# Performance work log

Measured on AMD Instinct MI355X. Metric: run time of the kernel, lower is better.

Reference implementation:

```python
import jax, jax.numpy as jnp
import numpy as np

D_MODEL, N_HEADS, D_FF, CTX_DIM = 512, 8, 2048, 20
D_K = D_MODEL // N_HEADS
SCALE = float(np.sqrt(D_K))
EPS = 1e-5


def _ln(x, g, b):
    mu = jnp.mean(x, axis=-1, keepdims=True)
    var = jnp.mean((x - mu) ** 2, axis=-1, keepdims=True)
    return (x - mu) * jax.lax.rsqrt(var + EPS) * g + b


def setup_inputs() -> dict:
    key = jax.random.key(0)
    ks = jax.random.split(key, 20)
    B, S = 2, 2048
    s = lambda d: 1.0 / np.sqrt(d)
    return {
        "x": jax.random.normal(ks[0], (B, S, D_MODEL), jnp.float32),
        "context": jax.random.normal(ks[1], (B, CTX_DIM), jnp.float32),
        "wq": jax.random.normal(ks[2], (D_MODEL, D_MODEL), jnp.float32) * s(D_MODEL),
        "wk": jax.random.normal(ks[3], (D_MODEL, D_MODEL), jnp.float32) * s(D_MODEL),
        "wv": jax.random.normal(ks[4], (D_MODEL, D_MODEL), jnp.float32) * s(D_MODEL),
        "wo": jax.random.normal(ks[5], (D_MODEL, D_MODEL), jnp.float32) * s(D_MODEL),
        "wo_b": jnp.zeros((D_MODEL,), jnp.float32),
        "wc": jax.random.normal(ks[6], (CTX_DIM, D_MODEL), jnp.float32) * s(CTX_DIM),
        "wc_b": jnp.zeros((D_MODEL,), jnp.float32),
        "wg": jax.random.normal(ks[7], (2 * D_MODEL, D_MODEL), jnp.float32) * s(2 * D_MODEL),
        "wg_b": jnp.zeros((D_MODEL,), jnp.float32),
        "opt_bias": jnp.zeros((N_HEADS, 1, 1), jnp.float32),
        "w1": jax.random.normal(ks[8], (D_MODEL, D_FF), jnp.float32) * s(D_MODEL),
        "b1": jnp.zeros((D_FF,), jnp.float32),
        "w2": jax.random.normal(ks[9], (D_FF, D_MODEL), jnp.float32) * s(D_FF),
        "b2": jnp.zeros((D_MODEL,), jnp.float32),
        "g1": jnp.ones((D_MODEL,), jnp.float32),
        "be1": jnp.zeros((D_MODEL,), jnp.float32),
        "g2": jnp.ones((D_MODEL,), jnp.float32),
        "be2": jnp.zeros((D_MODEL,), jnp.float32),
    }


def reference(x, context, wq, wk, wv, wo, wo_b, wc, wc_b, wg, wg_b, opt_bias,
              w1, b1, w2, b2, g1, be1, g2, be2):
    B, S, _ = x.shape
    # QKV projections -> [B, H, S, d_k]
    Q = (x @ wq).reshape(B, S, N_HEADS, D_K).transpose(0, 2, 1, 3)
    K = (x @ wk).reshape(B, S, N_HEADS, D_K).transpose(0, 2, 1, 3)
    V = (x @ wv).reshape(B, S, N_HEADS, D_K).transpose(0, 2, 1, 3)
    # scores [B, H, S, S] + learned per-head bias
    scores = jnp.einsum('bhqd,bhkd->bhqk', Q, K) / SCALE + opt_bias[None]
    # context-gated second score term
    ctx_proj = context @ wc + wc_b                      # [B, d_model]
    ctx_exp = jnp.broadcast_to(ctx_proj[:, None, :], (B, S, D_MODEL))
    combined = jnp.concatenate([x, ctx_exp], axis=-1)   # [B, S, 2*d_model]
    gate = jax.nn.sigmoid(combined @ wg + wg_b)         # [B, S, d_model]
    ctx_h = ctx_proj.reshape(B, N_HEADS, D_K)           # per-head context vectors
    ci = jnp.einsum('bhsd,bhd->bhs', Q, ctx_h) / SCALE  # [B, H, S]
    gate_h = gate.reshape(B, S, N_HEADS, D_K).mean(-1).transpose(0, 2, 1)  # [B, H, S]
    scores = scores + (ci * gate_h)[..., None]          # broadcast over keys
    attn = jax.nn.softmax(scores, axis=-1)
    ctx_out = jnp.einsum('bhqk,bhkd->bhqd', attn, V)
    ctx_out = ctx_out.transpose(0, 2, 1, 3).reshape(B, S, D_MODEL)
    attn_out = ctx_out @ wo + wo_b
    # residual + LN, FFN (exact GELU), residual + LN
    h = _ln(x + attn_out, g1, be1)
    ff = jax.nn.gelu(h @ w1 + b1, approximate=False) @ w2 + b2
    return _ln(h + ff, g2, be2)
```

## Files before the change

### kernel.cpp

```cpp
#include <hip/hip_runtime.h>
#include <hip/hip_bf16.h>
#include <math.h>

#define D_MODEL 512
#define N_HEADS 8
#define D_K     64
#define D_FF    2048
#define B_      2
#define S_      2048
#define M_TOT   (B_ * S_)

#define QSCALE  0.18033688011112042f

typedef __attribute__((ext_vector_type(8))) __bf16 bf16x8;
typedef __attribute__((ext_vector_type(4))) __bf16 bf16x4;
typedef __attribute__((ext_vector_type(4))) float  f32x4;
typedef __attribute__((ext_vector_type(4))) unsigned int u32x4;

static __device__ inline f32x4 mfma16(bf16x8 a, bf16x8 b, f32x4 c) {
    return __builtin_amdgcn_mfma_f32_16x16x32_bf16(a, b, c, 0, 0, 0);
}

static __device__ inline void gld_lds16(const __bf16* g, __bf16* l) {
    __builtin_amdgcn_global_load_lds(
        (const __attribute__((address_space(1))) void*)g,
        (__attribute__((address_space(3))) void*)l, 16, 0, 0);
}

static __device__ inline unsigned int pack_bf16(float a, float b) {
    union { __bf16 h; unsigned short u; } ua, ub;
    ua.h = (__bf16)a; ub.h = (__bf16)b;
    return (unsigned int)ua.u | ((unsigned int)ub.u << 16);
}

__global__ __launch_bounds__(256) void k_prep(const float* __restrict__ x,
                                              const float* __restrict__ wq,
                                              const float* __restrict__ wk,
                                              const float* __restrict__ wv,
                                              const float* __restrict__ wo,
                                              const float* __restrict__ w1,
                                              const float* __restrict__ w2,
                                              __bf16* __restrict__ xb,
                                              __bf16* __restrict__ wqkvT,
                                              __bf16* __restrict__ woT,
                                              __bf16* __restrict__ w1T,
                                              __bf16* __restrict__ w2T) {
    int bid = blockIdx.x, tid = threadIdx.x;
    if (bid < 2048) {
        int i = (bid * 256 + tid) * 4;
        float4 f = *(const float4*)(x + i);
        bf16x4 o = { (__bf16)f.x, (__bf16)f.y, (__bf16)f.z, (__bf16)f.w };
        *(bf16x4*)(xb + i) = o;
        return;
    }
    const float* W; __bf16* WT; int N, K, base;
    if (bid < 5120) {
        N = 512; K = 512;
        if (bid < 3072)      { W = wq; WT = wqkvT;          base = bid - 2048; }
        else if (bid < 4096) { W = wk; WT = wqkvT + 262144; base = bid - 3072; }
        else                 { W = wv; WT = wqkvT + 524288; base = bid - 4096; }
    } else if (bid < 6144)   { W = wo; WT = woT; N = 512;  K = 512;  base = bid - 5120; }
    else if (bid < 10240)    { W = w1; WT = w1T; N = 2048; K = 512;  base = bid - 6144; }
    else                     { W = w2; WT = w2T; N = 512;  K = 2048; base = bid - 10240; }
    int idx = base * 256 + tid;
    int k = idx / N, n = idx % N;
    WT[(size_t)n * K + k] = (__bf16)W[idx];
}

template<int BN, int MODE>
__global__ __launch_bounds__(256) void k_gemm128(const __bf16* __restrict__ A,
                                                 const __bf16* __restrict__ BT,
                                                 const float* __restrict__ bias,
                                                 void* __restrict__ out,
                                                 int M, int N, int K) {
    __shared__ __bf16 lds[(128 + BN) * 64];
    const int tid = threadIdx.x;
    const int lane = tid & 63, w = tid >> 6;
    const int lr = lane & 15, hi = lane >> 4;
    const int wm = w >> 1, wn = w & 1;
    const int bm0 = blockIdx.y * 128, bn0 = blockIdx.x * BN;
    constexpr int NT  = BN / 32;
    constexpr int BIT = BN / 32;
    f32x4 acc[4][NT] = {};

    for (int kt = 0; kt < K; kt += 64) {
#pragma unroll
        for (int a = 0; a < 4; a++) {
            int idx16 = a * 256 + tid;
            int r = idx16 >> 3, c8 = idx16 & 7;
            int k8 = c8 ^ (r & 7);
            gld_lds16(A + (size_t)(bm0 + r) * K + kt + k8 * 8,
                      (__bf16*)lds + (size_t)(a * 256 + w * 64) * 8);
        }
#pragma unroll
        for (int bq = 0; bq < BIT; bq++) {
            int idx16 = bq * 256 + tid;
            int r = idx16 >> 3, c8 = idx16 & 7;
            int k8 = c8 ^ (r & 7);
            gld_lds16(BT + (size_t)(bn0 + r) * K + kt + k8 * 8,
                      (__bf16*)lds + 128 * 64 + (size_t)(bq * 256 + w * 64) * 8);
        }
        __syncthreads();
#pragma unroll
        for (int kc = 0; kc < 2; kc++) {
            bf16x8 af[4], bf[NT];
#pragma unroll
            for (int mt = 0; mt < 4; mt++) {
                int r = wm * 64 + mt * 16 + lr;
                int c8 = (kc * 4 + hi) ^ (r & 7);
                af[mt] = *(const bf16x8*)&lds[r * 64 + c8 * 8];
            }
#pragma unroll
            for (int nt = 0; nt < NT; nt++) {
                int r = wn * (BN / 2) + nt * 16 + lr;
                int c8 = (kc * 4 + hi) ^ (r & 7);
                bf[nt] = *(const bf16x8*)&lds[128 * 64 + r * 64 + c8 * 8];
            }
#pragma unroll
            for (int mt = 0; mt < 4; mt++)
#pragma unroll
                for (int nt = 0; nt < NT; nt++)
                    acc[mt][nt] = mfma16(af[mt], bf[nt], acc[mt][nt]);
        }
        __syncthreads();
    }

#pragma unroll
    for (int mt = 0; mt < 4; mt++)
#pragma unroll
    for (int nt = 0; nt < NT; nt++)
#pragma unroll
    for (int i = 0; i < 4; i++) {
        int m = bm0 + wm * 64 + mt * 16 + hi * 4 + i;
        int n = bn0 + wn * (BN / 2) + nt * 16 + lr;
        float v = acc[mt][nt][i];
        if constexpr (MODE == 0) {
            int b = m >> 11, s = m & 2047;
            int seg = n >> 9, nn = n & 511;
            int h = nn >> 6, d = nn & 63;
            __bf16* base = (__bf16*)out;
            if (seg == 0)
                base[(((size_t)(b * N_HEADS + h)) * S_ + s) * D_K + d] = (__bf16)(v * QSCALE);
            else if (seg == 1)
                base[2097152 + (((size_t)(b * N_HEADS + h)) * S_ + s) * D_K + d] = (__bf16)v;
            else
                base[4194304 + (((size_t)(b * N_HEADS + h)) * D_K + d) * S_ + s] = (__bf16)v;
        } else if constexpr (MODE == 2) {
            v += bias[n];
            float gg = 0.5f * v * (1.0f + erff(v * 0.70710678118654752f));
            ((__bf16*)out)[(size_t)m * N + n] = (__bf16)gg;
        } else {
            ((float*)out)[(size_t)m * N + n] = v + bias[n];
        }
    }
}

__global__ __launch_bounds__(256) void k_attn2(const __bf16* __restrict__ Q,
                                               const __bf16* __restrict__ Kq,
                                               const __bf16* __restrict__ VT,
                                               __bf16* __restrict__ ctx) {
    const int lane = threadIdx.x & 63;
    const int w    = threadIdx.x >> 6;
    const int bh   = blockIdx.y;
    const int q0   = blockIdx.x * 64 + w * 16;
    const int lr   = lane & 15;
    const int hi   = lane >> 4;

    const __bf16* Qp = Q  + (size_t)bh * S_ * D_K;
    const __bf16* Kp = Kq + (size_t)bh * S_ * D_K;
    const __bf16* Vp = VT + (size_t)bh * D_K * S_;

    bf16x8 bq0 = *(const bf16x8*)&Qp[(size_t)(q0 + lr) * D_K + hi * 8];
    bf16x8 bq1 = *(const bf16x8*)&Qp[(size_t)(q0 + lr) * D_K + 32 + hi * 8];

    f32x4 acc[4] = {};
    float mrun = -1e30f, lrun = 0.0f;
    const int src0 = lr + ((hi & 1) << 5);
    const int src1 = src0 + 16;
    const bool csel = (hi & 2) != 0;

    for (int j = 0; j < S_; j += 64) {
        f32x4 sc[4] = {};
        __builtin_amdgcn_s_setprio(1);
#pragma unroll
        for (int c = 0; c < 4; c++) {
            bf16x8 ak0 = *(const bf16x8*)&Kp[(size_t)(j + c * 16 + lr) * D_K + hi * 8];
            bf16x8 ak1 = *(const bf16x8*)&Kp[(size_t)(j + c * 16 + lr) * D_K + 32 + hi * 8];
            sc[c] = mfma16(ak0, bq0, sc[c]);
            sc[c] = mfma16(ak1, bq1, sc[c]);
        }
        __builtin_amdgcn_s_setprio(0);
        float mt0 = fmaxf(fmaxf(sc[0][0], sc[0][1]), fmaxf(sc[0][2], sc[0][3]));
        float mt1 = fmaxf(fmaxf(sc[1][0], sc[1][1]), fmaxf(sc[1][2], sc[1][3]));
        float mt2 = fmaxf(fmaxf(sc[2][0], sc[2][1]), fmaxf(sc[2][2], sc[2][3]));
        float mt3 = fmaxf(fmaxf(sc[3][0], sc[3][1]), fmaxf(sc[3][2], sc[3][3]));
        float mt = fmaxf(fmaxf(mt0, mt1), fmaxf(mt2, mt3));
        mt = fmaxf(mt, __shfl_xor(mt, 16));
        mt = fmaxf(mt, __shfl_xor(mt, 32));
        float mnew = fmaxf(mrun, mt);
        float scl = exp2f(mrun - mnew);
        mrun = mnew;
        float p[4][4];
        float ps = 0.0f;
#pragma unroll
        for (int c = 0; c < 4; c++)
#pragma unroll
            for (int i = 0; i < 4; i++) {
                p[c][i] = exp2f(sc[c][i] - mnew);
                ps += p[c][i];
            }
        ps += __shfl_xor(ps, 16);
        ps += __shfl_xor(ps, 32);
        lrun = lrun * scl + ps;
        unsigned int pk[4][2];
#pragma unroll
        for (int c = 0; c < 4; c++) {
            pk[c][0] = pack_bf16(p[c][0], p[c][1]);
            pk[c][1] = pack_bf16(p[c][2], p[c][3]);
        }
        bf16x8 pb[2];
#pragma unroll
        for (int t = 0; t < 2; t++) {
            unsigned int d0a = __shfl((int)pk[2 * t][0],     src0);
            unsigned int d0b = __shfl((int)pk[2 * t + 1][0], src0);
            unsigned int d1a = __shfl((int)pk[2 * t][1],     src0);
            unsigned int d1b = __shfl((int)pk[2 * t + 1][1], src0);
            unsigned int d2a = __shfl((int)pk[2 * t][0],     src1);
            unsigned int d2b = __shfl((int)pk[2 * t + 1][0], src1);
            unsigned int d3a = __shfl((int)pk[2 * t][1],     src1);
            unsigned int d3b = __shfl((int)pk[2 * t + 1][1], src1);
            u32x4 u = { csel ? d0b : d0a, csel ? d1b : d1a,
                        csel ? d2b : d2a, csel ? d3b : d3a };
            pb[t] = __builtin_bit_cast(bf16x8, u);
        }
#pragma unroll
        for (int dt = 0; dt < 4; dt++)
#pragma unroll
            for (int i = 0; i < 4; i++) acc[dt][i] *= scl;
        __builtin_amdgcn_s_setprio(1);
#pragma unroll
        for (int dt = 0; dt < 4; dt++) {
            bf16x8 va0 = *(const bf16x8*)&Vp[(size_t)(dt * 16 + lr) * S_ + j + hi * 8];
            bf16x8 va1 = *(const bf16x8*)&Vp[(size_t)(dt * 16 + lr) * S_ + j + 32 + hi * 8];
            acc[dt] = mfma16(va0, pb[0], acc[dt]);
            acc[dt] = mfma16(va1, pb[1], acc[dt]);
        }
        __builtin_amdgcn_s_setprio(0);
    }

    float inv = 1.0f / lrun;
    int b = bh >> 3, h = bh & 7;
#pragma unroll
    for (int dt = 0; dt < 4; dt++) {
        bf16x4 o = { (__bf16)(acc[dt][0] * inv), (__bf16)(acc[dt][1] * inv),
                     (__bf16)(acc[dt][2] * inv), (__bf16)(acc[dt][3] * inv) };
        *(bf16x4*)&ctx[((size_t)(b * S_ + q0 + lr)) * D_MODEL + h * D_K + dt * 16 + hi * 4] = o;
    }
}

template<int WRITE_BF16>
__global__ __launch_bounds__(256) void k_ln(const float* __restrict__ base,
                                            const float* __restrict__ delta,
                                            const float* __restrict__ g,
                                            const float* __restrict__ be,
                                            float* __restrict__ outf,
                                            __bf16* __restrict__ outb) {
    int row  = blockIdx.x * 4 + (threadIdx.x >> 6);
    int lane = threadIdx.x & 63;
    const float4* A  = (const float4*)(base  + (size_t)row * D_MODEL);
    const float4* Bv = (const float4*)(delta + (size_t)row * D_MODEL);
    float4 a0 = A[lane],  a1 = A[lane + 64];
    float4 b0 = Bv[lane], b1 = Bv[lane + 64];
    float v[8] = { a0.x + b0.x, a0.y + b0.y, a0.z + b0.z, a0.w + b0.w,
                   a1.x + b1.x, a1.y + b1.y, a1.z + b1.z, a1.w + b1.w };
    float s1 = 0.0f, s2 = 0.0f;
#pragma unroll
    for (int j = 0; j < 8; j++) { s1 += v[j]; s2 += v[j] * v[j]; }
#pragma unroll
    for (int m = 1; m <= 32; m <<= 1) {
        s1 += __shfl_xor(s1, m);
        s2 += __shfl_xor(s2, m);
    }
    float mean = s1 * (1.0f / D_MODEL);
    float var  = s2 * (1.0f / D_MODEL) - mean * mean;
    float rstd = rsqrtf(var + 1e-5f);
    const float4* G  = (const float4*)g;
    const float4* Be = (const float4*)be;
    float4 g0 = G[lane],  g1v = G[lane + 64];
    float4 e0 = Be[lane], e1  = Be[lane + 64];
    float y[8];
    y[0] = (v[0] - mean) * rstd * g0.x  + e0.x;
    y[1] = (v[1] - mean) * rstd * g0.y  + e0.y;
    y[2] = (v[2] - mean) * rstd * g0.z  + e0.z;
    y[3] = (v[3] - mean) * rstd * g0.w  + e0.w;
    y[4] = (v[4] - mean) * rstd * g1v.x + e1.x;
    y[5] = (v[5] - mean) * rstd * g1v.y + e1.y;
    y[6] = (v[6] - mean) * rstd * g1v.z + e1.z;
    y[7] = (v[7] - mean) * rstd * g1v.w + e1.w;
    float4* O = (float4*)(outf + (size_t)row * D_MODEL);
    O[lane]      = make_float4(y[0], y[1], y[2], y[3]);
    O[lane + 64] = make_float4(y[4], y[5], y[6], y[7]);
    if constexpr (WRITE_BF16) {
        bf16x4 o0 = { (__bf16)y[0], (__bf16)y[1], (__bf16)y[2], (__bf16)y[3] };
        bf16x4 o1 = { (__bf16)y[4], (__bf16)y[5], (__bf16)y[6], (__bf16)y[7] };
        *(bf16x4*)&outb[(size_t)row * D_MODEL + lane * 4]       = o0;
        *(bf16x4*)&outb[(size_t)row * D_MODEL + 256 + lane * 4] = o1;
    }
}

extern "C" void kernel_launch(void* const* d_in, const int* in_sizes, int n_in,
                              void* d_out, int out_size, void* d_ws, size_t ws_size,
                              hipStream_t stream) {
    const float* x    = (const float*)d_in[0];
    const float* wq   = (const float*)d_in[2];
    const float* wk   = (const float*)d_in[3];
    const float* wv   = (const float*)d_in[4];
    const float* wo   = (const float*)d_in[5];
    const float* wo_b = (const float*)d_in[6];
    const float* w1   = (const float*)d_in[12];
    const float* b1   = (const float*)d_in[13];
    const float* w2   = (const float*)d_in[14];
    const float* b2   = (const float*)d_in[15];
    const float* g1   = (const float*)d_in[16];
    const float* be1  = (const float*)d_in[17];
    const float* g2   = (const float*)d_in[18];
    const float* be2  = (const float*)d_in[19];
    float* out = (float*)d_out;

    char* ws = (char*)d_ws;
    size_t off = 0;
    auto alloc = [&](size_t bytes) {
        void* p = ws + off;
        off += (bytes + 255) & ~(size_t)255;
        return p;
    };
    __bf16* xb    = (__bf16*)alloc((size_t)M_TOT * D_MODEL * 2);
    __bf16* wqkvT = (__bf16*)alloc((size_t)3 * D_MODEL * D_MODEL * 2);
    __bf16* woT   = (__bf16*)alloc((size_t)D_MODEL * D_MODEL * 2);
    __bf16* w1T   = (__bf16*)alloc((size_t)D_MODEL * D_FF * 2);
    __bf16* w2T   = (__bf16*)alloc((size_t)D_FF * D_MODEL * 2);
    __bf16* qkv   = (__bf16*)alloc((size_t)3 * M_TOT * D_MODEL * 2);
    __bf16* ctx   = (__bf16*)alloc((size_t)M_TOT * D_MODEL * 2);
    float*  aout  = (float*)alloc((size_t)M_TOT * D_MODEL * 4);
    float*  hf    = (float*)alloc((size_t)M_TOT * D_MODEL * 4);
    __bf16* hb    = (__bf16*)alloc((size_t)M_TOT * D_MODEL * 2);
    __bf16* ffb   = (__bf16*)alloc((size_t)M_TOT * D_FF * 2);
    float*  ff2   = (float*)alloc((size_t)M_TOT * D_MODEL * 4);
    (void)ws_size; (void)in_sizes; (void)n_in; (void)out_size;

    __bf16* Qb  = qkv;
    __bf16* Kb  = qkv + (size_t)M_TOT * D_MODEL;
    __bf16* VTb = qkv + (size_t)2 * M_TOT * D_MODEL;

    dim3 blk(256);
    k_prep<<<dim3(14336), blk, 0, stream>>>(x, wq, wk, wv, wo, w1, w2,
                                            xb, wqkvT, woT, w1T, w2T);
    k_gemm128<128, 0><<<dim3(12, 32), blk, 0, stream>>>(xb, wqkvT, nullptr, qkv,
                                                        M_TOT, 3 * D_MODEL, D_MODEL);
    k_attn2<<<dim3(S_ / 64, B_ * N_HEADS), blk, 0, stream>>>(Qb, Kb, VTb, ctx);
    k_gemm128<64, 1><<<dim3(8, 32), blk, 0, stream>>>(ctx, woT, wo_b, aout,
                                                      M_TOT, D_MODEL, D_MODEL);
    k_ln<1><<<dim3(M_TOT / 4), blk, 0, stream>>>(x, aout, g1, be1, hf, hb);
    k_gemm128<128, 2><<<dim3(16, 32), blk, 0, stream>>>(hb, w1T, b1, ffb,
                                                        M_TOT, D_FF, D_MODEL);
    k_gemm128<64, 3><<<dim3(8, 32), blk, 0, stream>>>(ffb, w2T, b2, ff2,
                                                      M_TOT, D_MODEL, D_FF);
    k_ln<0><<<dim3(M_TOT / 4), blk, 0, stream>>>(hf, ff2, g2, be2, out, nullptr);
}
```

Baseline: 337.4 us.

## Split attention over key range with combine kernel; tile weight transpose via LDS

Attention is split into four key-range partitions launched as a third grid dimension. Each writes unnormalized fp32 partial outputs plus running max and sum, and a new combine kernel merges them into the bf16 context. This raises the attention grid from 512 to 2048 blocks to fill more CUs, at the cost of extra fp32 partial traffic and an additional launch. Separately, the weight transpose in the prep kernel now uses 64x64 LDS tiles with coalesced vector loads and stores instead of scattered per-element writes.

Result: no change. 339.7 us (+0.7%).

```diff
diff --git a/kernel.cpp b/kernel.cpp
--- a/kernel.cpp
+++ b/kernel.cpp
@@ -9,6 +9,7 @@
 #define B_      2
 #define S_      2048
 #define M_TOT   (B_ * S_)
+#define NSPLIT  4
 
 #define QSCALE  0.18033688011112042f
 
@@ -53,18 +54,37 @@
         *(bf16x4*)(xb + i) = o;
         return;
     }
-    const float* W; __bf16* WT; int N, K, base;
-    if (bid < 5120) {
-        N = 512; K = 512;
-        if (bid < 3072)      { W = wq; WT = wqkvT;          base = bid - 2048; }
-        else if (bid < 4096) { W = wk; WT = wqkvT + 262144; base = bid - 3072; }
-        else                 { W = wv; WT = wqkvT + 524288; base = bid - 4096; }
-    } else if (bid < 6144)   { W = wo; WT = woT; N = 512;  K = 512;  base = bid - 5120; }
-    else if (bid < 10240)    { W = w1; WT = w1T; N = 2048; K = 512;  base = bid - 6144; }
-    else                     { W = w2; WT = w2T; N = 512;  K = 2048; base = bid - 10240; }
-    int idx = base * 256 + tid;
-    int k = idx / N, n = idx % N;
-    WT[(size_t)n * K + k] = (__bf16)W[idx];
+    __shared__ __bf16 t64[64 * 72];
+    int tt = bid - 2048;
+    const float* W; __bf16* WT; int N, K, ntiles, local;
+    if (tt < 256) {
+        N = 512; K = 512; ntiles = 8;
+        if (tt < 64)       { W = wq; WT = wqkvT;          local = tt; }
+        else if (tt < 128) { W = wk; WT = wqkvT + 262144; local = tt - 64; }
+        else if (tt < 192) { W = wv; WT = wqkvT + 524288; local = tt - 128; }
+        else               { W = wo; WT = woT;            local = tt - 192; }
+    } else if (tt < 512)   { W = w1; WT = w1T; N = 2048; K = 512;  ntiles = 32; local = tt - 256; }
+    else                   { W = w2; WT = w2T; N = 512;  K = 2048; ntiles = 8;  local = tt - 512; }
+    int k0 = (local / ntiles) * 64, n0 = (local % ntiles) * 64;
+
+#pragma unroll
+    for (int it = 0; it < 4; it++) {
+        int i = it * 256 + tid;
+        int r = i >> 4, c4 = i & 15;
+        float4 v = ((const float4*)(W + (size_t)(k0 + r) * N + n0))[c4];
+        t64[(c4 * 4 + 0) * 72 + r] = (__bf16)v.x;
+        t64[(c4 * 4 + 1) * 72 + r] = (__bf16)v.y;
+        t64[(c4 * 4 + 2) * 72 + r] = (__bf16)v.z;
+        t64[(c4 * 4 + 3) * 72 + r] = (__bf16)v.w;
+    }
+    __syncthreads();
+#pragma unroll
+    for (int it = 0; it < 2; it++) {
+        int j = it * 256 + tid;
+        int n = j >> 3, c8 = j & 7;
+        bf16x8 v = *(const bf16x8*)&t64[n * 72 + c8 * 8];
+        *(bf16x8*)&WT[(size_t)(n0 + n) * K + k0 + c8 * 8] = v;
+    }
 }
 
 template<int BN, int MODE>
@@ -155,13 +175,16 @@
     }
 }
 
-__global__ __launch_bounds__(256) void k_attn2(const __bf16* __restrict__ Q,
-                                               const __bf16* __restrict__ Kq,
-                                               const __bf16* __restrict__ VT,
-                                               __bf16* __restrict__ ctx) {
+__global__ __launch_bounds__(256, 8) void k_attn2(const __bf16* __restrict__ Q,
+                                                  const __bf16* __restrict__ Kq,
+                                                  const __bf16* __restrict__ VT,
+                                                  float* __restrict__ pO,
+                                                  float* __restrict__ pm,
+                                                  float* __restrict__ pl) {
     const int lane = threadIdx.x & 63;
     const int w    = threadIdx.x >> 6;
     const int bh   = blockIdx.y;
+    const int sp   = blockIdx.z;
     const int q0   = blockIdx.x * 64 + w * 16;
     const int lr   = lane & 15;
     const int hi   = lane >> 4;
@@ -179,7 +202,8 @@
     const int src1 = src0 + 16;
     const bool csel = (hi & 2) != 0;
 
-    for (int j = 0; j < S_; j += 64) {
+    const int j0 = sp * (S_ / NSPLIT);
+    for (int j = j0; j < j0 + S_ / NSPLIT; j += 64) {
         f32x4 sc[4] = {};
         __builtin_amdgcn_s_setprio(1);
 #pragma unroll
@@ -248,14 +272,43 @@
         __builtin_amdgcn_s_setprio(0);
     }
 
-    float inv = 1.0f / lrun;
+    float* pOw = pO + ((size_t)(sp * 16 + bh) * S_ + (q0 + lr)) * D_K;
+#pragma unroll
+    for (int dt = 0; dt < 4; dt++)
+        *(f32x4*)&pOw[dt * 16 + hi * 4] = acc[dt];
+    if (hi == 0) {
+        int idx = (sp * 16 + bh) * S_ + q0 + lr;
+        pm[idx] = mrun;
+        pl[idx] = lrun;
+    }
+}
+
+__global__ __launch_bounds__(256) void k_comb(const float* __restrict__ pO,
+                                              const float* __restrict__ pm,
+                                              const float* __restrict__ pl,
+                                              __bf16* __restrict__ ctx) {
+    int tid = threadIdx.x;
+    int d = tid & 63, r4 = tid >> 6;
+    int q = blockIdx.x * 4 + r4, bh = blockIdx.y;
+    float m[NSPLIT], l[NSPLIT];
+#pragma unroll
+    for (int sp = 0; sp < NSPLIT; sp++) {
+        int idx = (sp * 16 + bh) * S_ + q;
+        m[sp] = pm[idx];
+        l[sp] = pl[idx];
+    }
+    float ms = m[0];
+#pragma unroll
+    for (int sp = 1; sp < NSPLIT; sp++) ms = fmaxf(ms, m[sp]);
+    float ls = 0.0f, o = 0.0f;
+#pragma unroll
+    for (int sp = 0; sp < NSPLIT; sp++) {
+        float wsp = exp2f(m[sp] - ms);
+        ls += wsp * l[sp];
+        o  += wsp * pO[((size_t)(sp * 16 + bh) * S_ + q) * D_K + d];
+    }
     int b = bh >> 3, h = bh & 7;
-#pragma unroll
-    for (int dt = 0; dt < 4; dt++) {
-        bf16x4 o = { (__bf16)(acc[dt][0] * inv), (__bf16)(acc[dt][1] * inv),
-                     (__bf16)(acc[dt][2] * inv), (__bf16)(acc[dt][3] * inv) };
-        *(bf16x4*)&ctx[((size_t)(b * S_ + q0 + lr)) * D_MODEL + h * D_K + dt * 16 + hi * 4] = o;
-    }
+    ctx[((size_t)(b * S_ + q)) * D_MODEL + h * D_K + d] = (__bf16)(o / ls);
 }
 
 template<int WRITE_BF16>
@@ -346,6 +399,9 @@
     __bf16* hb    = (__bf16*)alloc((size_t)M_TOT * D_MODEL * 2);
     __bf16* ffb   = (__bf16*)alloc((size_t)M_TOT * D_FF * 2);
     float*  ff2   = (float*)alloc((size_t)M_TOT * D_MODEL * 4);
+    float*  pO    = (float*)alloc((size_t)NSPLIT * 16 * S_ * D_K * 4);
+    float*  pm    = (float*)alloc((size_t)NSPLIT * 16 * S_ * 4);
+    float*  pl    = (float*)alloc((size_t)NSPLIT * 16 * S_ * 4);
     (void)ws_size; (void)in_sizes; (void)n_in; (void)out_size;
 
     __bf16* Qb  = qkv;
@@ -353,11 +409,13 @@
     __bf16* VTb = qkv + (size_t)2 * M_TOT * D_MODEL;
 
     dim3 blk(256);
-    k_prep<<<dim3(14336), blk, 0, stream>>>(x, wq, wk, wv, wo, w1, w2,
-                                            xb, wqkvT, woT, w1T, w2T);
+    k_prep<<<dim3(2048 + 768), blk, 0, stream>>>(x, wq, wk, wv, wo, w1, w2,
+                                                 xb, wqkvT, woT, w1T, w2T);
     k_gemm128<128, 0><<<dim3(12, 32), blk, 0, stream>>>(xb, wqkvT, nullptr, qkv,
                                                         M_TOT, 3 * D_MODEL, D_MODEL);
-    k_attn2<<<dim3(S_ / 64, B_ * N_HEADS), blk, 0, stream>>>(Qb, Kb, VTb, ctx);
+    k_attn2<<<dim3(S_ / 64, B_ * N_HEADS, NSPLIT), blk, 0, stream>>>(Qb, Kb, VTb,
+                                                                     pO, pm, pl);
+    k_comb<<<dim3(S_ / 4, B_ * N_HEADS), blk, 0, stream>>>(pO, pm, pl, ctx);
     k_gemm128<64, 1><<<dim3(8, 32), blk, 0, stream>>>(ctx, woT, wo_b, aout,
                                                       M_TOT, D_MODEL, D_MODEL);
     k_ln<1><<<dim3(M_TOT / 4), blk, 0, stream>>>(x, aout, g1, be1, hf, hb);
```
